# Performance work log

Hardware: AMD Instinct MI355X
Metric: run time of the kernel (lower is better)

Reference implementation:

```python
import jax, jax.numpy as jnp
import numpy as np

A, M, H = 4, 1024, 1024
E, N = 8, 4096

def setup_inputs() -> dict:
    key = jax.random.key(0)
    kx, k1, k2 = jax.random.split(key, 3)
    x = jax.random.normal(kx, (A, M, H), dtype=jnp.float32)
    w1 = jax.random.normal(k1, (E, H, N), dtype=jnp.float32) * 0.02
    w2 = jax.random.normal(k2, (E, N, H), dtype=jnp.float32) * 0.02
    return {"x": x, "w1": w1, "w2": w2}

def reference(x, w1, w2):
    # mid: [A, E, M, N] = up-projection per expert
    mid = jnp.einsum('amh,ehn->aemn', x, w1)
    # down-projection per expert, then sum over experts e
    out = jnp.einsum('aemn,enh->amh', mid, w2)
    return out
```

## Files before the change

kernel.cpp:

```cpp
#include <hip/hip_runtime.h>
#include <hip/hip_bf16.h>
#include <stdint.h>


#define BN 128

typedef __attribute__((ext_vector_type(8))) short short8;
typedef __attribute__((ext_vector_type(4))) float float4v;
typedef __attribute__((ext_vector_type(4))) unsigned int uint4v;

__device__ __forceinline__ unsigned int rne_hi(unsigned int u) {
  return u + 0x7fffu + ((u >> 16) & 1u);
}

__device__ __forceinline__ unsigned int pack_bf16(float lo, float hi) {
  unsigned int ulo = rne_hi(__float_as_uint(lo));
  unsigned int uhi = rne_hi(__float_as_uint(hi));
  return __builtin_amdgcn_perm(uhi, ulo, 0x07060302u);
}

__device__ __forceinline__ void load_lds_16B(const void* g, void* lds) {
  __builtin_amdgcn_global_load_lds(
      (__attribute__((address_space(1))) void*)(uintptr_t)g,
      (__attribute__((address_space(3))) void*)(unsigned int)(uintptr_t)lds,
      16, 0, 0);
}


template <int MH, int NH>
__device__ __forceinline__ void mma_ph(float4v acc[8][4], const short8* aR,
                                       const short8 bR[2][4]) {
  __builtin_amdgcn_s_setprio(1);
#pragma unroll
  for (int fi = 0; fi < 4; ++fi)
#pragma unroll
    for (int fj = 0; fj < 2; ++fj)
#pragma unroll
      for (int s = 0; s < 2; ++s)
        acc[MH * 4 + fi][NH * 2 + fj] = __builtin_amdgcn_mfma_f32_16x16x32_bf16(
            aR[fi * 2 + s], bR[NH][fj * 2 + s], acc[MH * 4 + fi][NH * 2 + fj],
            0, 0, 0);
  __builtin_amdgcn_s_setprio(0);
}

template <bool ATOMIC>
__global__ __launch_bounds__(512, 2) void gemm1_8ph(
    const unsigned short* __restrict__ A, const unsigned short* __restrict__ Bt,
    float* __restrict__ C, long expStride, int ld, int Kc, int zdiv) {
  __shared__ __attribute__((aligned(16))) unsigned short As[2][2][128 * 64];
  __shared__ __attribute__((aligned(16))) unsigned short Bs[2][2][128 * 64];

  const int tid = threadIdx.x;
  const int wv = tid >> 6;
  const int ln = tid & 63;
  const int lrow = ln & 15;
  const int lq = ln >> 4;
  const int wmh = wv >> 2;
  const int wnq = wv & 3;
  const int breg = wnq >> 1;
  const int brow0 = (wnq & 1) * 64;

  const int nwg = gridDim.x;
  int wg = blockIdx.x;
  if ((nwg & 7) == 0) wg = (wg & 7) * (nwg >> 3) + (wg >> 3);
  const int tile = wg & 15;
  const int z = wg >> 4;
  const int e = z / zdiv;
  const int kc = z % zdiv;
  const int ty = tile >> 2, tx = tile & 3;

  const unsigned short* Ab =
      A + (long)e * expStride + (long)(ty * 256) * ld + (long)kc * Kc;
  const unsigned short* Bb =
      Bt + (long)e * expStride + (long)(tx * 256) * ld + (long)kc * Kc;

  const int srow = ln >> 3;
  const int scg = (ln & 7) ^ srow;

  auto stageA = [&](int b, int h, int kt) {
#pragma unroll
    for (int i = 0; i < 2; ++i) {
      const unsigned short* g =
          Ab + (long)(h * 128 + wv * 16 + i * 8 + srow) * ld + kt * 64 + scg * 8;
      load_lds_16B(g, (void*)&As[b][h][(wv * 2 + i) * 512]);
    }
  };
  auto stageB = [&](int b, int h, int kt) {
#pragma unroll
    for (int i = 0; i < 2; ++i) {
      const unsigned short* g =
          Bb + (long)(h * 128 + wv * 16 + i * 8 + srow) * ld + kt * 64 + scg * 8;
      load_lds_16B(g, (void*)&Bs[b][h][(wv * 2 + i) * 512]);
    }
  };

  float4v acc[8][4];
  float4v zero4 = {0.0f, 0.0f, 0.0f, 0.0f};
#pragma unroll
  for (int i = 0; i < 8; ++i)
#pragma unroll
    for (int j = 0; j < 4; ++j) acc[i][j] = zero4;

  short8 aR[8];
  short8 bR[2][4];

  auto ldsA = [&](int b, int mh) {
#pragma unroll
    for (int fi = 0; fi < 4; ++fi) {
      const int row = mh * 64 + fi * 16 + lrow;
#pragma unroll
      for (int s = 0; s < 2; ++s) {
        const int cg = (s * 4 + lq) ^ (row & 7);
        aR[fi * 2 + s] = *(const short8*)&As[b][wmh][row * 64 + cg * 8];
      }
    }
  };
  auto ldsB = [&](int b, int nh) {
#pragma unroll
    for (int fj = 0; fj < 2; ++fj) {
      const int row = brow0 + nh * 32 + fj * 16 + lrow;
#pragma unroll
      for (int s = 0; s < 2; ++s) {
        const int cg = (s * 4 + lq) ^ (row & 7);
        bR[nh][fj * 2 + s] = *(const short8*)&Bs[b][breg][row * 64 + cg * 8];
      }
    }
  };

  const int nkt = Kc / 64;

  stageA(0, 0, 0);
  stageA(0, 1, 0);
  stageB(0, 0, 0);
  stageB(0, 1, 0);
  stageA(1, 0, 1);
  stageA(1, 1, 1);
  stageB(1, 0, 1);
  stageB(1, 1, 1);
  asm volatile("s_waitcnt vmcnt(8)" ::: "memory");
  __builtin_amdgcn_s_barrier();

#define HALF_ITER(B, NN)                                            \
  {                                                                 \
    const int n2 = ((NN) + 2 < nkt) ? (NN) + 2 : nkt - 1;           \
    ldsA(B, 0);                                                     \
    ldsB(B, 0);                                                     \
    __builtin_amdgcn_s_barrier();                                   \
    asm volatile("s_waitcnt lgkmcnt(0)");                           \
    mma_ph<0, 0>(acc, aR, bR);                                      \
    __builtin_amdgcn_s_barrier();                                   \
    ldsB(B, 1);                                                     \
    __builtin_amdgcn_s_barrier();                                   \
    asm volatile("s_waitcnt lgkmcnt(0)");                           \
    mma_ph<0, 1>(acc, aR, bR);                                      \
    __builtin_amdgcn_s_barrier();                                   \
    ldsA(B, 1);                                                     \
    stageB(B, 0, n2);                                               \
    stageB(B, 1, n2);                                               \
    __builtin_amdgcn_s_barrier();                                   \
    asm volatile("s_waitcnt lgkmcnt(0)");                           \
    mma_ph<1, 1>(acc, aR, bR);                                      \
    __builtin_amdgcn_s_barrier();                                   \
    stageA(B, 0, n2);                                               \
    stageA(B, 1, n2);                                               \
    __builtin_amdgcn_s_barrier();                                   \
    mma_ph<1, 0>(acc, aR, bR);                                      \
    asm volatile("s_waitcnt vmcnt(8)" ::: "memory");                \
    __builtin_amdgcn_s_barrier();                                   \
  }

  for (int t = 0; t < nkt; t += 2) {
    HALF_ITER(0, t)
    HALF_ITER(1, t + 1)
  }
#undef HALF_ITER

  asm volatile("s_waitcnt vmcnt(0)" ::: "memory");

  float* Cz = ATOMIC ? C : C + (long)z * (1024L * 1024L);
  const int crow0 = ty * 256 + wmh * 128 + lq * 4;
  const int ccol0 = tx * 256 + wnq * 64 + lrow;
#pragma unroll
  for (int i = 0; i < 8; ++i)
#pragma unroll
    for (int j = 0; j < 4; ++j)
#pragma unroll
      for (int r = 0; r < 4; ++r) {
        const long idx = (long)(crow0 + i * 16 + r) * 1024 + ccol0 + j * 16;
        if (ATOMIC)
          atomicAdd(&Cz[idx], acc[i][j][r]);
        else
          Cz[idx] = acc[i][j][r];
      }
}

__global__ __launch_bounds__(256) void reduce16_cvt(
    const float* __restrict__ in, unsigned short* __restrict__ out) {
  const long i = ((long)blockIdx.x * 256 + threadIdx.x) * 4;
  float4 s = *(const float4*)(in + i);
#pragma unroll
  for (int zz = 1; zz < 16; ++zz) {
    float4 v = *(const float4*)(in + (long)zz * (1024L * 1024L) + i);
    s.x += v.x;
    s.y += v.y;
    s.z += v.z;
    s.w += v.w;
  }
  uint2 d;
  d.x = pack_bf16(s.x, s.y);
  d.y = pack_bf16(s.z, s.w);
  *(uint2*)(out + i) = d;
}

template <int MI, bool ATOMIC>
__global__ __launch_bounds__(256) void gemm_bf16(
    const unsigned short* __restrict__ A, int lda, long strideA,
    const unsigned short* __restrict__ Bt, int ldb, long strideB,
    float* __restrict__ C, int ldc, int K, int zdiv) {
  constexpr int BM = MI * 32;
  __shared__ __attribute__((aligned(16))) unsigned short As[2 * BM * 32];
  __shared__ __attribute__((aligned(16))) unsigned short Bs[2 * BN * 32];

  const int tid = threadIdx.x;
  const int wv = tid >> 6;
  const int ln = tid & 63;
  const int wm = (wv >> 1) * (MI * 16);
  const int wn = (wv & 1) * 64;
  const int lrow = ln & 15;
  const int lq = ln >> 4;
  const int sfrag = ((lq + (lrow >> 1)) & 3) * 16;

  const int zb = blockIdx.z / zdiv;
  const int zk = blockIdx.z % zdiv;
  const unsigned short* Ab = A + (long)zb * strideA + (long)zk * K +
                             (long)(blockIdx.y * BM) * lda;
  const unsigned short* Bb = Bt + (long)zb * strideB + (long)zk * K +
                             (long)(blockIdx.x * BN) * ldb;

  float4v zero4 = {0.0f, 0.0f, 0.0f, 0.0f};
  float4v acc[MI][4];
#pragma unroll
  for (int i = 0; i < MI; ++i)
#pragma unroll
    for (int j = 0; j < 4; ++j) acc[i][j] = zero4;

  const int nk = K / 64;
  for (int kt = 0; kt < nk; ++kt) {
    const int k0 = kt * 64;
    __syncthreads();
#pragma unroll
    for (int s = 0; s < 2; ++s) {
#pragma unroll
      for (int p = 0; p < BM / 64; ++p) {
        int o = p * 256 + wv * 64 + ln;
        int r = o >> 2;
        int gk = ((o & 3) - (r >> 1)) & 3;
        const unsigned short* g = Ab + (long)r * lda + k0 + s * 32 + gk * 8;
        char* lp = (char*)As + s * (BM * 64) + (p * 256 + wv * 64) * 16;
        load_lds_16B(g, lp);
      }
#pragma unroll
      for (int p = 0; p < 2; ++p) {
        int o = p * 256 + wv * 64 + ln;
        int r = o >> 2;
        int gk = ((o & 3) - (r >> 1)) & 3;
        const unsigned short* g = Bb + (long)r * ldb + k0 + s * 32 + gk * 8;
        char* lp = (char*)Bs + s * (BN * 64) + (p * 256 + wv * 64) * 16;
        load_lds_16B(g, lp);
      }
    }
    __syncthreads();

#pragma unroll
    for (int s = 0; s < 2; ++s) {
      short8 a[MI], b[4];
#pragma unroll
      for (int i = 0; i < MI; ++i)
        a[i] = *(const short8*)((const char*)As + s * (BM * 64) +
                                (wm + i * 16 + lrow) * 64 + sfrag);
#pragma unroll
      for (int j = 0; j < 4; ++j)
        b[j] = *(const short8*)((const char*)Bs + s * (BN * 64) +
                                (wn + j * 16 + lrow) * 64 + sfrag);
#pragma unroll
      for (int i = 0; i < MI; ++i)
#pragma unroll
        for (int j = 0; j < 4; ++j)
          acc[i][j] = __builtin_amdgcn_mfma_f32_16x16x32_bf16(a[i], b[j],
                                                              acc[i][j], 0, 0, 0);
    }
  }

  const int crow0 = blockIdx.y * BM + wm + lq * 4;
  const int ccol0 = blockIdx.x * BN + wn + lrow;
#pragma unroll
  for (int i = 0; i < MI; ++i)
#pragma unroll
    for (int j = 0; j < 4; ++j)
#pragma unroll
      for (int r = 0; r < 4; ++r) {
        int row = crow0 + i * 16 + r;
        int col = ccol0 + j * 16;
        if (ATOMIC)
          atomicAdd(&C[(long)row * ldc + col], acc[i][j][r]);
        else
          C[(long)row * ldc + col] = acc[i][j][r];
      }
}

__global__ __launch_bounds__(256) void cvt_f32_bf16(
    const float* __restrict__ in, unsigned short* __restrict__ out) {
  long i = ((long)blockIdx.x * 256 + threadIdx.x) * 8;
  float4 v0 = *(const float4*)(in + i);
  float4 v1 = *(const float4*)(in + i + 4);
  uint4v d;
  d.x = pack_bf16(v0.x, v0.y);
  d.y = pack_bf16(v0.z, v0.w);
  d.z = pack_bf16(v1.x, v1.y);
  d.w = pack_bf16(v1.z, v1.w);
  *(uint4v*)(out + i) = d;
}

__global__ __launch_bounds__(256) void transpose_cvt_kernel(
    const float* __restrict__ in, unsigned short* __restrict__ out,
    int R, int C, long strideBatch) {
  __shared__ float tile[64][65];
  const float* src = in + (long)blockIdx.z * strideBatch;
  unsigned short* dst = out + (long)blockIdx.z * strideBatch;
  const int t = threadIdx.x;
  const int c4 = (t & 15) * 4;
  const int r0 = t >> 4;
  const int by = blockIdx.y * 64;
  const int bx = blockIdx.x * 64;
#pragma unroll
  for (int p = 0; p < 4; ++p) {
    int r = r0 + p * 16;
    float4 v = *(const float4*)(src + (long)(by + r) * C + bx + c4);
    tile[r][c4 + 0] = v.x;
    tile[r][c4 + 1] = v.y;
    tile[r][c4 + 2] = v.z;
    tile[r][c4 + 3] = v.w;
  }
  __syncthreads();
#pragma unroll
  for (int p = 0; p < 4; ++p) {
    int cc = r0 + p * 16;
    int rr = c4;
    unsigned int d0 = pack_bf16(tile[rr + 0][cc], tile[rr + 1][cc]);
    unsigned int d1 = pack_bf16(tile[rr + 2][cc], tile[rr + 3][cc]);
    uint2 dd;
    dd.x = d0;
    dd.y = d1;
    *(uint2*)(dst + (long)(bx + cc) * R + by + rr) = dd;
  }
}

extern "C" void kernel_launch(void* const* d_in, const int* in_sizes, int n_in,
                              void* d_out, int out_size, void* d_ws, size_t ws_size,
                              hipStream_t stream) {
  const float* x = (const float*)d_in[0];
  const float* w1 = (const float*)d_in[1];
  const float* w2 = (const float*)d_in[2];
  float* out = (float*)d_out;

  const int A_ = 4, M_ = 1024, H_ = 1024, E_ = 8, N_ = 4096;
  const long EXP = (long)H_ * N_;

  const size_t base = (size_t)2 * E_ * EXP * 2 + (size_t)A_ * M_ * H_ * 2;
  const size_t need_part = base + 16ull * H_ * H_ * 4 + (size_t)H_ * H_ * 2;
  const size_t need_single = base + (size_t)H_ * H_ * 4 + (size_t)H_ * H_ * 2;

  if (ws_size >= need_part) {
    unsigned short* w2t = (unsigned short*)d_ws;
    unsigned short* w1b = w2t + (long)E_ * EXP;
    unsigned short* xb = w1b + (long)E_ * EXP;
    float* Wpart = (float*)(xb + (long)A_ * M_ * H_);
    unsigned short* Wb = (unsigned short*)(Wpart + 16L * H_ * H_);

    cvt_f32_bf16<<<(A_ * M_ * H_) / 2048, 256, 0, stream>>>(x, xb);
    transpose_cvt_kernel<<<dim3(H_ / 64, N_ / 64, E_), 256, 0, stream>>>(
        w2, w2t, N_, H_, EXP);
    cvt_f32_bf16<<<(int)(E_ * EXP / 2048), 256, 0, stream>>>(w1, w1b);

    gemm1_8ph<false><<<dim3(256), 512, 0, stream>>>(w2t, w1b, Wpart, EXP, N_,
                                                    N_ / 2, 2);
    reduce16_cvt<<<(H_ * H_) / 1024, 256, 0, stream>>>(Wpart, Wb);

    gemm_bf16<2, false><<<dim3(H_ / BN, (A_ * M_) / 64, 1), 256, 0, stream>>>(
        xb, H_, 0, Wb, H_, 0, out, H_, H_, 1);
  } else if (ws_size >= need_single) {
    unsigned short* w2t = (unsigned short*)d_ws;
    unsigned short* w1b = w2t + (long)E_ * EXP;
    unsigned short* xb = w1b + (long)E_ * EXP;
    float* Wacc = (float*)(xb + (long)A_ * M_ * H_);
    unsigned short* Wb = (unsigned short*)(Wacc + (long)H_ * H_);

    cvt_f32_bf16<<<(A_ * M_ * H_) / 2048, 256, 0, stream>>>(x, xb);
    transpose_cvt_kernel<<<dim3(H_ / 64, N_ / 64, E_), 256, 0, stream>>>(
        w2, w2t, N_, H_, EXP);
    cvt_f32_bf16<<<(int)(E_ * EXP / 2048), 256, 0, stream>>>(w1, w1b);
    hipMemsetAsync(Wacc, 0, (size_t)H_ * H_ * 4, stream);

    gemm1_8ph<true><<<dim3(256), 512, 0, stream>>>(w2t, w1b, Wacc, EXP, N_,
                                                   N_ / 2, 2);
    cvt_f32_bf16<<<(H_ * H_) / 2048, 256, 0, stream>>>(Wacc, Wb);

    gemm_bf16<2, false><<<dim3(H_ / BN, (A_ * M_) / 64, 1), 256, 0, stream>>>(
        xb, H_, 0, Wb, H_, 0, out, H_, H_, 1);
  } else {
    unsigned short* w2t = (unsigned short*)d_ws;
    unsigned short* w1b = w2t + 4 * EXP;
    unsigned short* xb = w1b + 4 * EXP;
    float* Wacc = (float*)(xb + (long)A_ * M_ * H_);
    unsigned short* Wb = (unsigned short*)(Wacc + (long)H_ * H_);

    cvt_f32_bf16<<<(A_ * M_ * H_) / 2048, 256, 0, stream>>>(x, xb);
    hipMemsetAsync(Wacc, 0, (size_t)H_ * H_ * 4, stream);

    for (int g = 0; g < 2; ++g) {
      const float* w2g = w2 + (long)g * 4 * EXP;
      const float* w1g = w1 + (long)g * 4 * EXP;
      transpose_cvt_kernel<<<dim3(H_ / 64, N_ / 64, 4), 256, 0, stream>>>(
          w2g, w2t, N_, H_, EXP);
      cvt_f32_bf16<<<(int)(4 * EXP / 2048), 256, 0, stream>>>(w1g, w1b);
      gemm1_8ph<true><<<dim3(256), 512, 0, stream>>>(w2t, w1b, Wacc, EXP, N_,
                                                     N_ / 4, 4);
    }

    cvt_f32_bf16<<<(H_ * H_) / 2048, 256, 0, stream>>>(Wacc, Wb);
    gemm_bf16<2, false><<<dim3(H_ / BN, (A_ * M_) / 64, 1), 256, 0, stream>>>(
        xb, H_, 0, Wb, H_, 0, out, H_, H_, 1);
  }
}
```

Before: 402.6 us.

## Fuse w1 fp32-to-bf16 conversion into weight-product GEMM B-operand loads

Removes the separate pass that converted w1 to bf16 and instead reads fp32 w1 directly in the first GEMM, packing it to bf16 in registers before writing to LDS. Staging switches from async global-to-LDS loads to register-staged loads for both operands, with prefetch issued early and LDS writes placed between MFMA phases. This saves a full read and write of the converted w1 plus a kernel launch. In exchange the GEMM reads twice the bytes for B, uses more VGPRs, and gives up the direct-to-LDS load path.

```diff
diff --git a/kernel.cpp b/kernel.cpp
--- a/kernel.cpp
+++ b/kernel.cpp
@@ -26,7 +26,6 @@
       16, 0, 0);
 }
 
-
 template <int MH, int NH>
 __device__ __forceinline__ void mma_ph(float4v acc[8][4], const short8* aR,
                                        const short8 bR[2][4]) {
@@ -45,7 +44,7 @@
 
 template <bool ATOMIC>
 __global__ __launch_bounds__(512, 2) void gemm1_8ph(
-    const unsigned short* __restrict__ A, const unsigned short* __restrict__ Bt,
+    const unsigned short* __restrict__ A, const float* __restrict__ Bf,
     float* __restrict__ C, long expStride, int ld, int Kc, int zdiv) {
   __shared__ __attribute__((aligned(16))) unsigned short As[2][2][128 * 64];
   __shared__ __attribute__((aligned(16))) unsigned short Bs[2][2][128 * 64];
@@ -71,27 +70,54 @@
 
   const unsigned short* Ab =
       A + (long)e * expStride + (long)(ty * 256) * ld + (long)kc * Kc;
-  const unsigned short* Bb =
-      Bt + (long)e * expStride + (long)(tx * 256) * ld + (long)kc * Kc;
+  const float* Bb =
+      Bf + (long)e * expStride + (long)(tx * 256) * ld + (long)kc * Kc;
 
   const int srow = ln >> 3;
   const int scg = (ln & 7) ^ srow;
 
-  auto stageA = [&](int b, int h, int kt) {
-#pragma unroll
-    for (int i = 0; i < 2; ++i) {
-      const unsigned short* g =
-          Ab + (long)(h * 128 + wv * 16 + i * 8 + srow) * ld + kt * 64 + scg * 8;
-      load_lds_16B(g, (void*)&As[b][h][(wv * 2 + i) * 512]);
-    }
-  };
-  auto stageB = [&](int b, int h, int kt) {
-#pragma unroll
-    for (int i = 0; i < 2; ++i) {
-      const unsigned short* g =
-          Bb + (long)(h * 128 + wv * 16 + i * 8 + srow) * ld + kt * 64 + scg * 8;
-      load_lds_16B(g, (void*)&Bs[b][h][(wv * 2 + i) * 512]);
-    }
+  short8 av[2][2];
+  float4 bv[2][2][2];
+
+  auto issueA = [&](int kt) {
+#pragma unroll
+    for (int h = 0; h < 2; ++h)
+#pragma unroll
+      for (int i = 0; i < 2; ++i)
+        av[h][i] = *(const short8*)(Ab +
+                                    (long)(h * 128 + wv * 16 + i * 8 + srow) * ld +
+                                    kt * 64 + scg * 8);
+  };
+  auto issueB = [&](int kt) {
+#pragma unroll
+    for (int h = 0; h < 2; ++h)
+#pragma unroll
+      for (int i = 0; i < 2; ++i) {
+        const float* g = Bb + (long)(h * 128 + wv * 16 + i * 8 + srow) * ld +
+                         kt * 64 + scg * 8;
+        bv[h][i][0] = *(const float4*)(g);
+        bv[h][i][1] = *(const float4*)(g + 4);
+      }
+  };
+  auto writeA = [&](int b) {
+#pragma unroll
+    for (int h = 0; h < 2; ++h)
+#pragma unroll
+      for (int i = 0; i < 2; ++i)
+        *(short8*)&As[b][h][(wv * 2 + i) * 512 + ln * 8] = av[h][i];
+  };
+  auto writeB = [&](int b) {
+#pragma unroll
+    for (int h = 0; h < 2; ++h)
+#pragma unroll
+      for (int i = 0; i < 2; ++i) {
+        uint4v d;
+        d.x = pack_bf16(bv[h][i][0].x, bv[h][i][0].y);
+        d.y = pack_bf16(bv[h][i][0].z, bv[h][i][0].w);
+        d.z = pack_bf16(bv[h][i][1].x, bv[h][i][1].y);
+        d.w = pack_bf16(bv[h][i][1].z, bv[h][i][1].w);
+        *(uint4v*)&Bs[b][h][(wv * 2 + i) * 512 + ln * 8] = d;
+      }
   };
 
   float4v acc[8][4];
@@ -129,43 +155,46 @@
 
   const int nkt = Kc / 64;
 
-  stageA(0, 0, 0);
-  stageA(0, 1, 0);
-  stageB(0, 0, 0);
-  stageB(0, 1, 0);
-  stageA(1, 0, 1);
-  stageA(1, 1, 1);
-  stageB(1, 0, 1);
-  stageB(1, 1, 1);
-  asm volatile("s_waitcnt vmcnt(8)" ::: "memory");
+  issueA(0);
+  issueB(0);
+  writeA(0);
+  writeB(0);
+  issueA(1);
+  issueB(1);
+  writeA(1);
+  writeB(1);
+  asm volatile("s_waitcnt lgkmcnt(0)" ::: "memory");
   __builtin_amdgcn_s_barrier();
 
 #define HALF_ITER(B, NN)                                            \
   {                                                                 \
-    const int n2 = ((NN) + 2 < nkt) ? (NN) + 2 : nkt - 1;           \
+    const int n2 = (NN) + 2;                                        \
+    const bool doPre = n2 < nkt;                                    \
     ldsA(B, 0);                                                     \
     ldsB(B, 0);                                                     \
-    __builtin_amdgcn_s_barrier();                                   \
-    asm volatile("s_waitcnt lgkmcnt(0)");                           \
+    if (doPre) {                                                    \
+      issueA(n2);                                                   \
+      issueB(n2);                                                   \
+    }                                                               \
+    __builtin_amdgcn_s_barrier();                                   \
+    asm volatile("s_waitcnt lgkmcnt(0)" ::: "memory");              \
     mma_ph<0, 0>(acc, aR, bR);                                      \
     __builtin_amdgcn_s_barrier();                                   \
     ldsB(B, 1);                                                     \
     __builtin_amdgcn_s_barrier();                                   \
-    asm volatile("s_waitcnt lgkmcnt(0)");                           \
+    asm volatile("s_waitcnt lgkmcnt(0)" ::: "memory");              \
     mma_ph<0, 1>(acc, aR, bR);                                      \
     __builtin_amdgcn_s_barrier();                                   \
     ldsA(B, 1);                                                     \
-    stageB(B, 0, n2);                                               \
-    stageB(B, 1, n2);                                               \
-    __builtin_amdgcn_s_barrier();                                   \
-    asm volatile("s_waitcnt lgkmcnt(0)");                           \
+    if (doPre) writeB(B);                                           \
+    __builtin_amdgcn_s_barrier();                                   \
+    asm volatile("s_waitcnt lgkmcnt(0)" ::: "memory");              \
     mma_ph<1, 1>(acc, aR, bR);                                      \
     __builtin_amdgcn_s_barrier();                                   \
-    stageA(B, 0, n2);                                               \
-    stageA(B, 1, n2);                                               \
+    if (doPre) writeA(B);                                           \
     __builtin_amdgcn_s_barrier();                                   \
     mma_ph<1, 0>(acc, aR, bR);                                      \
-    asm volatile("s_waitcnt vmcnt(8)" ::: "memory");                \
+    asm volatile("s_waitcnt lgkmcnt(0)" ::: "memory");              \
     __builtin_amdgcn_s_barrier();                                   \
   }
 
@@ -174,8 +203,6 @@
     HALF_ITER(1, t + 1)
   }
 #undef HALF_ITER
-
-  asm volatile("s_waitcnt vmcnt(0)" ::: "memory");
 
   float* Cz = ATOMIC ? C : C + (long)z * (1024L * 1024L);
   const int crow0 = ty * 256 + wmh * 128 + lq * 4;
@@ -366,23 +393,23 @@
   const int A_ = 4, M_ = 1024, H_ = 1024, E_ = 8, N_ = 4096;
   const long EXP = (long)H_ * N_;
 
-  const size_t base = (size_t)2 * E_ * EXP * 2 + (size_t)A_ * M_ * H_ * 2;
-  const size_t need_part = base + 16ull * H_ * H_ * 4 + (size_t)H_ * H_ * 2;
-  const size_t need_single = base + (size_t)H_ * H_ * 4 + (size_t)H_ * H_ * 2;
+  const size_t wsA8 = (size_t)E_ * EXP * 2;
+  const size_t wsA4 = (size_t)4 * EXP * 2;
+  const size_t wsX = (size_t)A_ * M_ * H_ * 2;
+  const size_t need_part = wsA8 + wsX + 16ull * H_ * H_ * 4 + (size_t)H_ * H_ * 2;
+  const size_t need_single = wsA8 + wsX + (size_t)H_ * H_ * 4 + (size_t)H_ * H_ * 2;
 
   if (ws_size >= need_part) {
     unsigned short* w2t = (unsigned short*)d_ws;
-    unsigned short* w1b = w2t + (long)E_ * EXP;
-    unsigned short* xb = w1b + (long)E_ * EXP;
+    unsigned short* xb = w2t + (long)E_ * EXP;
     float* Wpart = (float*)(xb + (long)A_ * M_ * H_);
     unsigned short* Wb = (unsigned short*)(Wpart + 16L * H_ * H_);
 
     cvt_f32_bf16<<<(A_ * M_ * H_) / 2048, 256, 0, stream>>>(x, xb);
     transpose_cvt_kernel<<<dim3(H_ / 64, N_ / 64, E_), 256, 0, stream>>>(
         w2, w2t, N_, H_, EXP);
-    cvt_f32_bf16<<<(int)(E_ * EXP / 2048), 256, 0, stream>>>(w1, w1b);
-
-    gemm1_8ph<false><<<dim3(256), 512, 0, stream>>>(w2t, w1b, Wpart, EXP, N_,
+
+    gemm1_8ph<false><<<dim3(256), 512, 0, stream>>>(w2t, w1, Wpart, EXP, N_,
                                                     N_ / 2, 2);
     reduce16_cvt<<<(H_ * H_) / 1024, 256, 0, stream>>>(Wpart, Wb);
 
@@ -390,18 +417,16 @@
         xb, H_, 0, Wb, H_, 0, out, H_, H_, 1);
   } else if (ws_size >= need_single) {
     unsigned short* w2t = (unsigned short*)d_ws;
-    unsigned short* w1b = w2t + (long)E_ * EXP;
-    unsigned short* xb = w1b + (long)E_ * EXP;
+    unsigned short* xb = w2t + (long)E_ * EXP;
     float* Wacc = (float*)(xb + (long)A_ * M_ * H_);
     unsigned short* Wb = (unsigned short*)(Wacc + (long)H_ * H_);
 
     cvt_f32_bf16<<<(A_ * M_ * H_) / 2048, 256, 0, stream>>>(x, xb);
     transpose_cvt_kernel<<<dim3(H_ / 64, N_ / 64, E_), 256, 0, stream>>>(
         w2, w2t, N_, H_, EXP);
-    cvt_f32_bf16<<<(int)(E_ * EXP / 2048), 256, 0, stream>>>(w1, w1b);
     hipMemsetAsync(Wacc, 0, (size_t)H_ * H_ * 4, stream);
 
-    gemm1_8ph<true><<<dim3(256), 512, 0, stream>>>(w2t, w1b, Wacc, EXP, N_,
+    gemm1_8ph<true><<<dim3(256), 512, 0, stream>>>(w2t, w1, Wacc, EXP, N_,
                                                    N_ / 2, 2);
     cvt_f32_bf16<<<(H_ * H_) / 2048, 256, 0, stream>>>(Wacc, Wb);
 
@@ -409,8 +434,7 @@
         xb, H_, 0, Wb, H_, 0, out, H_, H_, 1);
   } else {
     unsigned short* w2t = (unsigned short*)d_ws;
-    unsigned short* w1b = w2t + 4 * EXP;
-    unsigned short* xb = w1b + 4 * EXP;
+    unsigned short* xb = w2t + wsA4 / 2;
     float* Wacc = (float*)(xb + (long)A_ * M_ * H_);
     unsigned short* Wb = (unsigned short*)(Wacc + (long)H_ * H_);
 
@@ -422,8 +446,7 @@
       const float* w1g = w1 + (long)g * 4 * EXP;
       transpose_cvt_kernel<<<dim3(H_ / 64, N_ / 64, 4), 256, 0, stream>>>(
           w2g, w2t, N_, H_, EXP);
-      cvt_f32_bf16<<<(int)(4 * EXP / 2048), 256, 0, stream>>>(w1g, w1b);
-      gemm1_8ph<true><<<dim3(256), 512, 0, stream>>>(w2t, w1b, Wacc, EXP, N_,
+      gemm1_8ph<true><<<dim3(256), 512, 0, stream>>>(w2t, w1g, Wacc, EXP, N_,
                                                      N_ / 4, 4);
     }
 
```

After: 536.1 us. 1.33x slower.
